# Kernel tuning notes

Hardware: AMD Instinct MI355X
Metric: run time of the kernel (lower is better)

Reference implementation:

```python
import jax, jax.numpy as jnp
import numpy as np

N_NODES = 50000
N_EDGES = 500000
H = 128          # h_dim
HEADS = 3
B = 512          # histories with non-zero length
L = 10           # seq_len (all histories full length)
N_RELS = 200
NEG_SLOPE = 0.2  # DGL GATConv default negative_slope


def setup_inputs() -> dict:
    key = jax.random.key(0)
    ks = jax.random.split(key, 18)
    p = lambda i, shape: jax.random.normal(ks[i], shape, jnp.float32) * 0.05
    return {
        "node_feat": jax.random.normal(ks[0], (N_NODES, H), jnp.float32),
        "W1": p(1, (H, HEADS * H)),
        "attn_l1": p(2, (HEADS, H)),
        "attn_r1": p(3, (HEADS, H)),
        "b1": p(4, (HEADS * H,)),
        "W2": p(5, (H, HEADS * H)),
        "attn_l2": p(6, (HEADS, H)),
        "attn_r2": p(7, (HEADS, H)),
        "b2": p(8, (HEADS * H,)),
        "ent_embeds": jax.random.normal(ks[9], (N_NODES, H), jnp.float32),
        "rel_embeds": jax.random.normal(ks[10], (N_RELS, H), jnp.float32),
        "global_emb_list": jax.random.normal(ks[11], (B * L, H), jnp.float32),
        "s_hist_t": jax.random.uniform(ks[12], (B, L), jnp.float32),
        "edge_src": jax.random.randint(ks[13], (N_EDGES,), 0, N_NODES),
        "edge_dst": jax.random.randint(ks[14], (N_EDGES,), 0, N_NODES),
        "node_ids_graph": jax.random.randint(ks[15], (B * L,), 0, N_NODES),
        "s_tem": jax.random.randint(ks[16], (B,), 0, N_NODES),
        "r_tem": jax.random.randint(ks[17], (B,), 0, N_RELS),
    }


def gat_conv(x, W, attn_l, attn_r, bias, src, dst):
    """DGL-style GATConv (allow_zero_in_degree=True, eval mode)."""
    n = x.shape[0]
    feat = (x @ W).reshape(n, HEADS, H)                    # [N, heads, H]
    el = jnp.einsum('nhd,hd->nh', feat, attn_l)            # [N, heads]
    er = jnp.einsum('nhd,hd->nh', feat, attn_r)
    e = jax.nn.leaky_relu(el[src] + er[dst], NEG_SLOPE)    # [E, heads]
    # edge softmax over incoming edges of each dst node
    emax = jax.ops.segment_max(e, dst, num_segments=n)
    ex = jnp.exp(e - emax[dst])
    denom = jax.ops.segment_sum(ex, dst, num_segments=n)
    alpha = ex / denom[dst]                                # [E, heads]
    msg = alpha[:, :, None] * feat[src]                    # [E, heads, H]
    rst = jax.ops.segment_sum(msg, dst, num_segments=n)    # [N, heads, H]
    return rst + bias.reshape(1, HEADS, H)


def reference(node_feat, W1, attn_l1, attn_r1, b1, W2, attn_l2, attn_r2, b2,
              ent_embeds, rel_embeds, global_emb_list, s_hist_t,
              edge_src, edge_dst, node_ids_graph, s_tem, r_tem):
    h = gat_conv(node_feat, W1, attn_l1, attn_r1, b1, edge_src, edge_dst).mean(axis=1)
    h = gat_conv(h, W2, attn_l2, attn_r2, b2, edge_src, edge_dst).mean(axis=1)
    embeds = h[node_ids_graph].reshape(B, L, H)            # gathered history node embeds
    ent = jnp.broadcast_to(ent_embeds[s_tem][:, None, :], (B, L, H))
    rel = jnp.broadcast_to(rel_embeds[r_tem][:, None, :], (B, L, H))
    glob = global_emb_list.reshape(B, L, H)
    seq = jnp.concatenate([embeds, ent, rel, glob], axis=-1)   # [B, L, 4H]
    seq_r = jnp.concatenate([embeds, ent, glob], axis=-1)      # [B, L, 3H]
    return seq, seq_r, s_hist_t
```

## Files before the change

### kernel.cpp

```cpp
#include <hip/hip_runtime.h>
#include <hip/hip_bf16.h>

#define N_NODES 50000
#define N_EDGES 500000
#define HDIM 128
#define HEADS 3
#define BB 512
#define LL 10
#define NEG_SLOPE 0.2f

typedef __hip_bfloat16 bf16;
typedef unsigned char fp8t;
typedef __bf16 v8bf __attribute__((ext_vector_type(8)));
typedef float f32x4 __attribute__((ext_vector_type(4)));


__global__ void k_zero2(int* a, int na, int* b, int nb){
  int i = blockIdx.x*256 + threadIdx.x;
  if(i < na) a[i] = 0;
  if(i < nb) b[i] = 0;
}

__global__ void k_hist(const int* __restrict__ dst, int* __restrict__ cnt, int E){
  int e = blockIdx.x*256 + threadIdx.x;
  if(e < E) atomicAdd(&cnt[dst[e]], 1);
}

__global__ void k_cvt(const float* __restrict__ in, bf16* __restrict__ o, int n){
  int i = (blockIdx.x*256 + threadIdx.x)*8;
  if(i < n){
    f32x4 lo = *reinterpret_cast<const f32x4*>(in + i);
    f32x4 hi = *reinterpret_cast<const f32x4*>(in + i + 4);
    v8bf v;
    #pragma unroll
    for(int j = 0; j < 4; ++j){ v[j] = (__bf16)lo[j]; v[4+j] = (__bf16)hi[j]; }
    *reinterpret_cast<v8bf*>(o + i) = v;
  }
}


#define SCAN_TILE 2048
#define SCAN_NB ((N_NODES + SCAN_TILE - 1)/SCAN_TILE)

__global__ __launch_bounds__(256) void k_scan_part(const int* __restrict__ cnt,
                                                   int* __restrict__ bsum){
  int b = blockIdx.x, tid = threadIdx.x;
  int i0 = b*SCAN_TILE + tid*8;
  int s = 0;
  #pragma unroll
  for(int j = 0; j < 8; ++j){ int i = i0 + j; s += (i < N_NODES) ? cnt[i] : 0; }
  for(int m = 32; m; m >>= 1) s += __shfl_xor(s, m);
  __shared__ int ws[4];
  if((tid & 63) == 0) ws[tid >> 6] = s;
  __syncthreads();
  if(tid == 0) bsum[b] = ws[0] + ws[1] + ws[2] + ws[3];
}

__global__ __launch_bounds__(64) void k_scan_top(int* __restrict__ bsum, int nb){
  int tid = threadIdx.x;
  int v = (tid < nb) ? bsum[tid] : 0;
  for(int s = 1; s < 64; s <<= 1){
    int t = __shfl_up(v, s);
    if(tid >= s) v += t;
  }
  if(tid < nb) bsum[tid] = v;
}

__global__ __launch_bounds__(256) void k_scan_write(int* __restrict__ cnt,
                                                    const int* __restrict__ bsum,
                                                    int* __restrict__ offs){
  int b = blockIdx.x, tid = threadIdx.x;
  int lane = tid & 63, wv = tid >> 6;
  int i0 = b*SCAN_TILE + tid*8;
  int v[8]; int s = 0;
  #pragma unroll
  for(int j = 0; j < 8; ++j){
    int i = i0 + j;
    v[j] = (i < N_NODES) ? cnt[i] : 0;
    s += v[j];
  }
  #pragma unroll
  for(int j = 0; j < 8; ++j){ int i = i0 + j; if(i < N_NODES) cnt[i] = 0; }
  int incl = s;
  for(int sh = 1; sh < 64; sh <<= 1){
    int t = __shfl_up(incl, sh);
    if(lane >= sh) incl += t;
  }
  __shared__ int wtot[4];
  if(lane == 63) wtot[wv] = incl;
  __syncthreads();
  int woff = 0;
  for(int w = 0; w < wv; ++w) woff += wtot[w];
  int excl = woff + incl - s;
  int run = ((b > 0) ? bsum[b-1] : 0) + excl;
  #pragma unroll
  for(int j = 0; j < 8; ++j){
    int i = i0 + j;
    run += v[j];
    if(i < N_NODES) offs[i+1] = run;
  }
  if(b == 0 && tid == 0) offs[0] = 0;
}

__global__ void k_scatter(const int* __restrict__ src, const int* __restrict__ dst,
                          const int* __restrict__ offs, int* __restrict__ cur,
                          int* __restrict__ csr, int E){
  int e = blockIdx.x*256 + threadIdx.x;
  if(e < E){
    int d = dst[e];
    int p = offs[d] + atomicAdd(&cur[d], 1);
    if(p >= 0 && p < E) csr[p] = src[e];
  }
}


__global__ __launch_bounds__(64) void k_mark(const int* __restrict__ nid,
                                             const int* __restrict__ offs,
                                             const int* __restrict__ csr,
                                             unsigned char* __restrict__ mark){
  unsigned n = (unsigned)nid[blockIdx.x];
  if(n >= N_NODES) return;
  if(threadIdx.x == 0) mark[n] = 1;
  int o0 = offs[n], o1 = offs[n+1];
  for(int j = o0 + (int)threadIdx.x; j < o1; j += 64){
    unsigned s = (unsigned)csr[j];
    if(s < N_NODES) mark[s] = 1;
  }
}


__global__ void k_wt(const float* __restrict__ W, bf16* __restrict__ Wt){
  int i = blockIdx.x*256 + threadIdx.x;
  if(i < HEADS*HDIM*HDIM){
    int n = i >> 7, k = i & 127;
    Wt[i] = __float2bfloat16(W[k*(HEADS*HDIM) + n]);
  }
}


__global__ __launch_bounds__(256) void k_gemm(const bf16* __restrict__ A,
                                              const bf16* __restrict__ Wt,
                                              const float* __restrict__ al,
                                              const float* __restrict__ ar,
                                              fp8t* __restrict__ feat8,
                                              float* __restrict__ el4,
                                              float* __restrict__ er4, int M){
  int tid  = threadIdx.x;
  int wave = tid >> 6, lane = tid & 63;
  int wr = wave >> 1, wc = wave & 1;
  int row0 = blockIdx.x*64 + wr*32;
  int col0 = blockIdx.y*128 + wc*64;
  int l15 = lane & 15, lhi = lane >> 4;

  v8bf a[4][2], b[4][4];
  #pragma unroll
  for(int kk = 0; kk < 4; ++kk){
    int kb = kk*32 + lhi*8;
    #pragma unroll
    for(int mi = 0; mi < 2; ++mi){
      int r = row0 + mi*16 + l15;
      if(r >= M) r = M - 1;
      a[kk][mi] = *reinterpret_cast<const v8bf*>(A + (size_t)r*HDIM + kb);
    }
    #pragma unroll
    for(int ni = 0; ni < 4; ++ni){
      int c = col0 + ni*16 + l15;
      b[kk][ni] = *reinterpret_cast<const v8bf*>(Wt + (size_t)c*HDIM + kb);
    }
  }

  f32x4 acc[2][4] = {};
  #pragma unroll
  for(int kk = 0; kk < 4; ++kk)
    #pragma unroll
    for(int mi = 0; mi < 2; ++mi)
      #pragma unroll
      for(int ni = 0; ni < 4; ++ni)
        acc[mi][ni] = __builtin_amdgcn_mfma_f32_16x16x32_bf16(a[kk][mi], b[kk][ni],
                                                              acc[mi][ni], 0, 0, 0);

  const float* alh = al + blockIdx.y*HDIM;
  const float* arh = ar + blockIdx.y*HDIM;
  float alv[4], arv[4];
  #pragma unroll
  for(int ni = 0; ni < 4; ++ni){
    int d = wc*64 + ni*16 + l15;
    alv[ni] = alh[d]; arv[ni] = arh[d];
  }
  __shared__ float red[2][64][2];
  __shared__ int4 tile4[512];
  fp8t* tile8 = (fp8t*)tile4;

  #pragma unroll
  for(int mi = 0; mi < 2; ++mi){
    #pragma unroll
    for(int j = 0; j < 4; ++j){
      float pe = 0.f, pr = 0.f;
      #pragma unroll
      for(int ni = 0; ni < 4; ++ni){
        pe += acc[mi][ni][j]*alv[ni];
        pr += acc[mi][ni][j]*arv[ni];
      }
      for(int k = 8; k; k >>= 1){ pe += __shfl_xor(pe, k); pr += __shfl_xor(pr, k); }
      int row_l = wr*32 + mi*16 + lhi*4 + j;
      if(l15 == 0){ red[wc][row_l][0] = pe; red[wc][row_l][1] = pr; }
    }
  }
  #pragma unroll
  for(int mi = 0; mi < 2; ++mi)
    #pragma unroll
    for(int j = 0; j < 4; ++j){
      int row_l = wr*32 + mi*16 + lhi*4 + j;
      #pragma unroll
      for(int ni = 0; ni < 4; ++ni){
        float x = acc[mi][ni][j];
        unsigned bb = (unsigned)__builtin_amdgcn_cvt_pk_fp8_f32(x, x, 0, false) & 0xFFu;
        tile8[row_l*128 + wc*64 + ni*16 + l15] = (fp8t)bb;
      }
    }
  __syncthreads();

  if(tid < 64){
    int r = blockIdx.x*64 + tid;
    if(r < M){
      el4[(size_t)r*4 + blockIdx.y] = red[0][tid][0] + red[1][tid][0];
      er4[(size_t)r*4 + blockIdx.y] = red[0][tid][1] + red[1][tid][1];
    }
  }
  #pragma unroll
  for(int pass = 0; pass < 2; ++pass){
    int off = pass*4096 + tid*16;
    int row_l = off >> 7, col = off & 127;
    int r = blockIdx.x*64 + row_l;
    if(r < M)
      *reinterpret_cast<int4*>(feat8 + (size_t)r*(HEADS*HDIM) + blockIdx.y*HDIM + col) =
          tile4[off >> 4];
  }
}


__device__ __forceinline__ float lrelu(float x){ return x > 0.f ? x : NEG_SLOPE*x; }

#define AGG_CHUNK 128
#define SEQ_SZ   (BB*LL*4*HDIM)
#define SEQR_OFF SEQ_SZ
#define SEQR_SZ  (BB*LL*3*HDIM)
#define SH_OFF   (SEQ_SZ + SEQR_SZ)

template<int USE_LIST, int FUSED, int USE_MARK>
__global__ __launch_bounds__(128) void k_agg(const fp8t* __restrict__ feat8,
                                             const float* __restrict__ el4,
                                             const float* __restrict__ er4,
                                             const float* __restrict__ bias,
                                             const int* __restrict__ offs,
                                             const int* __restrict__ csr,
                                             const int* __restrict__ list,
                                             const unsigned char* __restrict__ mark,
                                             bf16* __restrict__ h1,
                                             const float* __restrict__ ent_e,
                                             const float* __restrict__ rel_e,
                                             const float* __restrict__ glob,
                                             const float* __restrict__ sht,
                                             const int* __restrict__ s_tem,
                                             const int* __restrict__ r_tem,
                                             float* __restrict__ out){
  int bid = blockIdx.x;
  int n = USE_LIST ? list[bid] : bid;
  if(USE_MARK){ if(!mark[n]) return; }
  int tid = threadIdx.x;
  __shared__ float s_alpha[AGG_CHUNK][4];
  __shared__ int   s_src[AGG_CHUNK];
  __shared__ float s_facc[HEADS*HDIM];
  int o0 = offs[n];
  int deg = offs[n+1] - o0;
  if(deg < 0 || deg > N_EDGES) deg = 0;
  float4 erv = *reinterpret_cast<const float4*>(er4 + (size_t)n*4);

  float a0 = 0.f, a1 = 0.f, a2 = 0.f, a3 = 0.f, dh = 0.f;
  int head = tid >> 5;
  for(int base = 0; base < deg; base += AGG_CHUNK){
    int cn = min(AGG_CHUNK, deg - base);
    if(base) __syncthreads();
    if(tid < cn){
      unsigned su = (unsigned)csr[o0 + base + tid];
      if(su >= N_NODES) su = 0;
      float4 elv = *reinterpret_cast<const float4*>(el4 + (size_t)su*4);
      s_src[tid] = (int)su;
      s_alpha[tid][0] = __expf(lrelu(elv.x + erv.x));
      s_alpha[tid][1] = __expf(lrelu(elv.y + erv.y));
      s_alpha[tid][2] = __expf(lrelu(elv.z + erv.z));
    }
    __syncthreads();
    if(tid < 96){
      for(int i = 0; i < cn; ++i){
        unsigned u = *reinterpret_cast<const unsigned*>(
            feat8 + (size_t)s_src[i]*(HEADS*HDIM) + tid*4);
        float al = s_alpha[i][head];
        dh += al;
        a0 += al*__builtin_amdgcn_cvt_f32_fp8((int)u, 0);
        a1 += al*__builtin_amdgcn_cvt_f32_fp8((int)u, 1);
        a2 += al*__builtin_amdgcn_cvt_f32_fp8((int)u, 2);
        a3 += al*__builtin_amdgcn_cvt_f32_fp8((int)u, 3);
      }
    }
  }
  if(tid < 96){
    float inv = (dh > 0.f) ? 1.f/dh : 0.f;
    float4 w; w.x = a0*inv; w.y = a1*inv; w.z = a2*inv; w.w = a3*inv;
    *reinterpret_cast<float4*>(s_facc + tid*4) = w;
  }
  __syncthreads();
  float r = (s_facc[tid] + s_facc[HDIM + tid] + s_facc[2*HDIM + tid]
           + bias[tid] + bias[HDIM + tid] + bias[2*HDIM + tid])*(1.f/3.f);
  if(FUSED){
    int p = bid, b = p/LL, d = tid;
    float ent = ent_e[(size_t)s_tem[b]*HDIM + d];
    float rel = rel_e[(size_t)r_tem[b]*HDIM + d];
    float gl  = glob[(size_t)p*HDIM + d];
    size_t so = (size_t)p*(4*HDIM);
    out[so + d] = r; out[so + HDIM + d] = ent;
    out[so + 2*HDIM + d] = rel; out[so + 3*HDIM + d] = gl;
    size_t ro = SEQR_OFF + (size_t)p*(3*HDIM);
    out[ro + d] = r; out[ro + HDIM + d] = ent; out[ro + 2*HDIM + d] = gl;
    if(d == 0) out[SH_OFF + p] = sht[p];
  } else {
    h1[(size_t)n*HDIM + tid] = __float2bfloat16(r);
  }
}


extern "C" void kernel_launch(void* const* d_in, const int* in_sizes, int n_in,
                              void* d_out, int out_size, void* d_ws, size_t ws_size,
                              hipStream_t stream){
  const float* node_feat = (const float*)d_in[0];
  const float* W1        = (const float*)d_in[1];
  const float* attn_l1   = (const float*)d_in[2];
  const float* attn_r1   = (const float*)d_in[3];
  const float* b1        = (const float*)d_in[4];
  const float* W2        = (const float*)d_in[5];
  const float* attn_l2   = (const float*)d_in[6];
  const float* attn_r2   = (const float*)d_in[7];
  const float* b2        = (const float*)d_in[8];
  const float* ent_emb   = (const float*)d_in[9];
  const float* rel_emb   = (const float*)d_in[10];
  const float* glob      = (const float*)d_in[11];
  const float* sht       = (const float*)d_in[12];
  const int*  e_src      = (const int*)d_in[13];
  const int*  e_dst      = (const int*)d_in[14];
  const int*  nid        = (const int*)d_in[15];
  const int*  s_tem      = (const int*)d_in[16];
  const int*  r_tem      = (const int*)d_in[17];
  float* out = (float*)d_out;

  char* ws = (char*)d_ws;
  size_t cur_off = 0;
  auto alloc = [&](size_t bytes)->char*{
    char* r = ws + cur_off;
    cur_off += (bytes + 255) & ~(size_t)255;
    return r;
  };
  fp8t*  feat8 = (fp8t*) alloc((size_t)N_NODES*HEADS*HDIM);
  bf16*  nfb   = (bf16*) alloc((size_t)N_NODES*HDIM*2);
  bf16*  h1    = (bf16*) alloc((size_t)N_NODES*HDIM*2);
  float* el4   = (float*)alloc((size_t)N_NODES*4*4);
  float* er4   = (float*)alloc((size_t)N_NODES*4*4);
  bf16*  wt1   = (bf16*) alloc((size_t)HEADS*HDIM*HDIM*2);
  bf16*  wt2   = (bf16*) alloc((size_t)HEADS*HDIM*HDIM*2);
  int*   offs  = (int*)  alloc((size_t)(N_NODES+1)*4);
  int*   cnt   = (int*)  alloc((size_t)N_NODES*4);
  int*   bsum  = (int*)  alloc((size_t)SCAN_NB*4);
  unsigned char* mark = (unsigned char*)alloc((size_t)N_NODES);
  int*   csr   = (int*)  alloc((size_t)N_EDGES*4);

  k_zero2<<<(N_NODES+255)/256, 256, 0, stream>>>(cnt, N_NODES,
                                                 (int*)mark, (N_NODES+3)/4);
  k_hist<<<(N_EDGES+255)/256, 256, 0, stream>>>(e_dst, cnt, N_EDGES);
  k_scan_part<<<SCAN_NB, 256, 0, stream>>>(cnt, bsum);
  k_scan_top<<<1, 64, 0, stream>>>(bsum, SCAN_NB);
  k_scan_write<<<SCAN_NB, 256, 0, stream>>>(cnt, bsum, offs);
  k_scatter<<<(N_EDGES+255)/256, 256, 0, stream>>>(e_src, e_dst, offs, cnt, csr, N_EDGES);
  k_mark<<<BB*LL, 64, 0, stream>>>(nid, offs, csr, mark);

  k_wt<<<(HEADS*HDIM*HDIM+255)/256, 256, 0, stream>>>(W1, wt1);
  k_wt<<<(HEADS*HDIM*HDIM+255)/256, 256, 0, stream>>>(W2, wt2);
  k_cvt<<<(N_NODES*HDIM/8+255)/256, 256, 0, stream>>>(node_feat, nfb, N_NODES*HDIM);

  dim3 ggrid((N_NODES + 63)/64, HEADS);

  k_gemm<<<ggrid, 256, 0, stream>>>(nfb, wt1, attn_l1, attn_r1,
                                    feat8, el4, er4, N_NODES);
  k_agg<0,0,1><<<N_NODES, 128, 0, stream>>>(feat8, el4, er4, b1, offs, csr,
                                            nullptr, mark, h1,
                                            nullptr, nullptr, nullptr, nullptr,
                                            nullptr, nullptr, nullptr);

  k_gemm<<<ggrid, 256, 0, stream>>>(h1, wt2, attn_l2, attn_r2,
                                    feat8, el4, er4, N_NODES);
  k_agg<1,1,0><<<BB*LL, 128, 0, stream>>>(feat8, el4, er4, b2, offs, csr,
                                          nid, nullptr, nullptr,
                                          ent_emb, rel_emb, glob, sht,
                                          s_tem, r_tem, out);
}
```

Baseline: 197.4 us.

## Compact marked nodes for layer-2 GEMM and use wave-per-node aggregation

Builds a compacted list of the nodes needed by the final gather, from the existing mark array, using an atomic counter. The second-layer GEMM then computes projections only for those listed rows and exits early for blocks beyond the count. The aggregation kernel is also rewritten from one 128-thread block per node with shared-memory staging and barriers to one 64-lane wave per node, with four waves per block. Per-edge weights are broadcast through wave shuffles and the output uses vectorized stores. The compaction costs an extra kernel and an atomic, and list order is nondeterministic but only changes which row goes where.

```diff
diff --git a/kernel.cpp b/kernel.cpp
--- a/kernel.cpp
+++ b/kernel.cpp
@@ -15,10 +15,11 @@
 typedef float f32x4 __attribute__((ext_vector_type(4)));
 
 
-__global__ void k_zero2(int* a, int na, int* b, int nb){
+__global__ void k_zero2(int* a, int na, int* b, int nb, int* c){
   int i = blockIdx.x*256 + threadIdx.x;
   if(i < na) a[i] = 0;
   if(i < nb) b[i] = 0;
+  if(i == 0) c[0] = 0;
 }
 
 __global__ void k_hist(const int* __restrict__ dst, int* __restrict__ cnt, int E){
@@ -128,6 +129,15 @@
   }
 }
 
+__global__ void k_mklist(const unsigned char* __restrict__ mark,
+                         int* __restrict__ list, int* __restrict__ cnt){
+  int i = blockIdx.x*256 + threadIdx.x;
+  if(i < N_NODES && mark[i]){
+    int p = atomicAdd(cnt, 1);
+    list[p] = i;
+  }
+}
+
 
 __global__ void k_wt(const float* __restrict__ W, bf16* __restrict__ Wt){
   int i = blockIdx.x*256 + threadIdx.x;
@@ -138,13 +148,19 @@
 }
 
 
+template<int LIST>
 __global__ __launch_bounds__(256) void k_gemm(const bf16* __restrict__ A,
                                               const bf16* __restrict__ Wt,
                                               const float* __restrict__ al,
                                               const float* __restrict__ ar,
                                               fp8t* __restrict__ feat8,
                                               float* __restrict__ el4,
-                                              float* __restrict__ er4, int M){
+                                              float* __restrict__ er4,
+                                              const int* __restrict__ list,
+                                              const int* __restrict__ pcnt,
+                                              int M){
+  int Meff = LIST ? pcnt[0] : M;
+  if(blockIdx.x*64 >= Meff) return;
   int tid  = threadIdx.x;
   int wave = tid >> 6, lane = tid & 63;
   int wr = wave >> 1, wc = wave & 1;
@@ -153,15 +169,19 @@
   int l15 = lane & 15, lhi = lane >> 4;
 
   v8bf a[4][2], b[4][4];
+  int nodeA[2];
+  #pragma unroll
+  for(int mi = 0; mi < 2; ++mi){
+    int r = row0 + mi*16 + l15;
+    if(r >= Meff) r = Meff - 1;
+    nodeA[mi] = LIST ? list[r] : r;
+  }
   #pragma unroll
   for(int kk = 0; kk < 4; ++kk){
     int kb = kk*32 + lhi*8;
     #pragma unroll
-    for(int mi = 0; mi < 2; ++mi){
-      int r = row0 + mi*16 + l15;
-      if(r >= M) r = M - 1;
-      a[kk][mi] = *reinterpret_cast<const v8bf*>(A + (size_t)r*HDIM + kb);
-    }
+    for(int mi = 0; mi < 2; ++mi)
+      a[kk][mi] = *reinterpret_cast<const v8bf*>(A + (size_t)nodeA[mi]*HDIM + kb);
     #pragma unroll
     for(int ni = 0; ni < 4; ++ni){
       int c = col0 + ni*16 + l15;
@@ -222,9 +242,10 @@
 
   if(tid < 64){
     int r = blockIdx.x*64 + tid;
-    if(r < M){
-      el4[(size_t)r*4 + blockIdx.y] = red[0][tid][0] + red[1][tid][0];
-      er4[(size_t)r*4 + blockIdx.y] = red[0][tid][1] + red[1][tid][1];
+    if(r < Meff){
+      int node = LIST ? list[r] : r;
+      el4[(size_t)node*4 + blockIdx.y] = red[0][tid][0] + red[1][tid][0];
+      er4[(size_t)node*4 + blockIdx.y] = red[0][tid][1] + red[1][tid][1];
     }
   }
   #pragma unroll
@@ -232,23 +253,24 @@
     int off = pass*4096 + tid*16;
     int row_l = off >> 7, col = off & 127;
     int r = blockIdx.x*64 + row_l;
-    if(r < M)
-      *reinterpret_cast<int4*>(feat8 + (size_t)r*(HEADS*HDIM) + blockIdx.y*HDIM + col) =
+    if(r < Meff){
+      int node = LIST ? list[r] : r;
+      *reinterpret_cast<int4*>(feat8 + (size_t)node*(HEADS*HDIM) + blockIdx.y*HDIM + col) =
           tile4[off >> 4];
+    }
   }
 }
 
 
 __device__ __forceinline__ float lrelu(float x){ return x > 0.f ? x : NEG_SLOPE*x; }
 
-#define AGG_CHUNK 128
 #define SEQ_SZ   (BB*LL*4*HDIM)
 #define SEQR_OFF SEQ_SZ
 #define SEQR_SZ  (BB*LL*3*HDIM)
 #define SH_OFF   (SEQ_SZ + SEQR_SZ)
 
 template<int USE_LIST, int FUSED, int USE_MARK>
-__global__ __launch_bounds__(128) void k_agg(const fp8t* __restrict__ feat8,
+__global__ __launch_bounds__(256) void k_agg(const fp8t* __restrict__ feat8,
                                              const float* __restrict__ el4,
                                              const float* __restrict__ er4,
                                              const float* __restrict__ bias,
@@ -263,68 +285,100 @@
                                              const float* __restrict__ sht,
                                              const int* __restrict__ s_tem,
                                              const int* __restrict__ r_tem,
-                                             float* __restrict__ out){
-  int bid = blockIdx.x;
-  int n = USE_LIST ? list[bid] : bid;
+                                             float* __restrict__ out,
+                                             int total){
+  int widx = blockIdx.x*4 + (threadIdx.x >> 6);
+  int lane = threadIdx.x & 63;
+  if(widx >= total) return;
+  int n = USE_LIST ? list[widx] : widx;
   if(USE_MARK){ if(!mark[n]) return; }
-  int tid = threadIdx.x;
-  __shared__ float s_alpha[AGG_CHUNK][4];
-  __shared__ int   s_src[AGG_CHUNK];
-  __shared__ float s_facc[HEADS*HDIM];
   int o0 = offs[n];
   int deg = offs[n+1] - o0;
   if(deg < 0 || deg > N_EDGES) deg = 0;
   float4 erv = *reinterpret_cast<const float4*>(er4 + (size_t)n*4);
 
-  float a0 = 0.f, a1 = 0.f, a2 = 0.f, a3 = 0.f, dh = 0.f;
-  int head = tid >> 5;
-  for(int base = 0; base < deg; base += AGG_CHUNK){
-    int cn = min(AGG_CHUNK, deg - base);
-    if(base) __syncthreads();
-    if(tid < cn){
-      unsigned su = (unsigned)csr[o0 + base + tid];
+  float aA0=0.f,aA1=0.f,aA2=0.f,aA3=0.f, dhA=0.f;
+  float aB0=0.f,aB1=0.f,aB2=0.f,aB3=0.f, dhB=0.f;
+  int headA = lane >> 5;
+
+  for(int base = 0; base < deg; base += 64){
+    int cn = min(64, deg - base);
+    float e0 = 0.f, e1 = 0.f, e2 = 0.f; int s = 0;
+    if(lane < cn){
+      unsigned su = (unsigned)csr[o0 + base + lane];
       if(su >= N_NODES) su = 0;
+      s = (int)su;
       float4 elv = *reinterpret_cast<const float4*>(el4 + (size_t)su*4);
-      s_src[tid] = (int)su;
-      s_alpha[tid][0] = __expf(lrelu(elv.x + erv.x));
-      s_alpha[tid][1] = __expf(lrelu(elv.y + erv.y));
-      s_alpha[tid][2] = __expf(lrelu(elv.z + erv.z));
-    }
-    __syncthreads();
-    if(tid < 96){
-      for(int i = 0; i < cn; ++i){
-        unsigned u = *reinterpret_cast<const unsigned*>(
-            feat8 + (size_t)s_src[i]*(HEADS*HDIM) + tid*4);
-        float al = s_alpha[i][head];
-        dh += al;
-        a0 += al*__builtin_amdgcn_cvt_f32_fp8((int)u, 0);
-        a1 += al*__builtin_amdgcn_cvt_f32_fp8((int)u, 1);
-        a2 += al*__builtin_amdgcn_cvt_f32_fp8((int)u, 2);
-        a3 += al*__builtin_amdgcn_cvt_f32_fp8((int)u, 3);
+      e0 = __expf(lrelu(elv.x + erv.x));
+      e1 = __expf(lrelu(elv.y + erv.y));
+      e2 = __expf(lrelu(elv.z + erv.z));
+    }
+    for(int i = 0; i < cn; ++i){
+      int  si = __shfl(s,  i);
+      float b0 = __shfl(e0, i);
+      float b1 = __shfl(e1, i);
+      float b2 = __shfl(e2, i);
+      const fp8t* fr = feat8 + (size_t)si*(HEADS*HDIM);
+      unsigned uA = *reinterpret_cast<const unsigned*>(fr + lane*4);
+      float alA = headA ? b1 : b0;
+      dhA += alA;
+      aA0 += alA*__builtin_amdgcn_cvt_f32_fp8((int)uA, 0);
+      aA1 += alA*__builtin_amdgcn_cvt_f32_fp8((int)uA, 1);
+      aA2 += alA*__builtin_amdgcn_cvt_f32_fp8((int)uA, 2);
+      aA3 += alA*__builtin_amdgcn_cvt_f32_fp8((int)uA, 3);
+      if(lane < 32){
+        unsigned uB = *reinterpret_cast<const unsigned*>(fr + 256 + lane*4);
+        dhB += b2;
+        aB0 += b2*__builtin_amdgcn_cvt_f32_fp8((int)uB, 0);
+        aB1 += b2*__builtin_amdgcn_cvt_f32_fp8((int)uB, 1);
+        aB2 += b2*__builtin_amdgcn_cvt_f32_fp8((int)uB, 2);
+        aB3 += b2*__builtin_amdgcn_cvt_f32_fp8((int)uB, 3);
       }
     }
   }
-  if(tid < 96){
-    float inv = (dh > 0.f) ? 1.f/dh : 0.f;
-    float4 w; w.x = a0*inv; w.y = a1*inv; w.z = a2*inv; w.w = a3*inv;
-    *reinterpret_cast<float4*>(s_facc + tid*4) = w;
-  }
-  __syncthreads();
-  float r = (s_facc[tid] + s_facc[HDIM + tid] + s_facc[2*HDIM + tid]
-           + bias[tid] + bias[HDIM + tid] + bias[2*HDIM + tid])*(1.f/3.f);
-  if(FUSED){
-    int p = bid, b = p/LL, d = tid;
-    float ent = ent_e[(size_t)s_tem[b]*HDIM + d];
-    float rel = rel_e[(size_t)r_tem[b]*HDIM + d];
-    float gl  = glob[(size_t)p*HDIM + d];
-    size_t so = (size_t)p*(4*HDIM);
-    out[so + d] = r; out[so + HDIM + d] = ent;
-    out[so + 2*HDIM + d] = rel; out[so + 3*HDIM + d] = gl;
-    size_t ro = SEQR_OFF + (size_t)p*(3*HDIM);
-    out[ro + d] = r; out[ro + HDIM + d] = ent; out[ro + 2*HDIM + d] = gl;
-    if(d == 0) out[SH_OFF + p] = sht[p];
-  } else {
-    h1[(size_t)n*HDIM + tid] = __float2bfloat16(r);
+
+  float invA = (dhA > 0.f) ? 1.f/dhA : 0.f;
+  float invB = (dhB > 0.f) ? 1.f/dhB : 0.f;
+  float nA0 = aA0*invA, nA1 = aA1*invA, nA2 = aA2*invA, nA3 = aA3*invA;
+  float x0 = __shfl(nA0, lane + 32);
+  float x1 = __shfl(nA1, lane + 32);
+  float x2 = __shfl(nA2, lane + 32);
+  float x3 = __shfl(nA3, lane + 32);
+  if(lane < 32){
+    int m = lane;
+    float4 bs0 = *reinterpret_cast<const float4*>(bias + 4*m);
+    float4 bs1 = *reinterpret_cast<const float4*>(bias + HDIM + 4*m);
+    float4 bs2 = *reinterpret_cast<const float4*>(bias + 2*HDIM + 4*m);
+    float4 r;
+    r.x = (nA0 + x0 + aB0*invB + bs0.x + bs1.x + bs2.x)*(1.f/3.f);
+    r.y = (nA1 + x1 + aB1*invB + bs0.y + bs1.y + bs2.y)*(1.f/3.f);
+    r.z = (nA2 + x2 + aB2*invB + bs0.z + bs1.z + bs2.z)*(1.f/3.f);
+    r.w = (nA3 + x3 + aB3*invB + bs0.w + bs1.w + bs2.w)*(1.f/3.f);
+    if(FUSED){
+      int p = widx, bb = p/LL;
+      float4 ent = *reinterpret_cast<const float4*>(ent_e + (size_t)s_tem[bb]*HDIM + 4*m);
+      float4 rel = *reinterpret_cast<const float4*>(rel_e + (size_t)r_tem[bb]*HDIM + 4*m);
+      float4 gl  = *reinterpret_cast<const float4*>(glob + (size_t)p*HDIM + 4*m);
+      float* so = out + (size_t)p*(4*HDIM) + 4*m;
+      *reinterpret_cast<float4*>(so)            = r;
+      *reinterpret_cast<float4*>(so + HDIM)     = ent;
+      *reinterpret_cast<float4*>(so + 2*HDIM)   = rel;
+      *reinterpret_cast<float4*>(so + 3*HDIM)   = gl;
+      float* ro = out + SEQR_OFF + (size_t)p*(3*HDIM) + 4*m;
+      *reinterpret_cast<float4*>(ro)            = r;
+      *reinterpret_cast<float4*>(ro + HDIM)     = ent;
+      *reinterpret_cast<float4*>(ro + 2*HDIM)   = gl;
+      if(m == 0) out[SH_OFF + p] = sht[p];
+    } else {
+      bf16 t0 = __float2bfloat16(r.x), t1 = __float2bfloat16(r.y);
+      bf16 t2 = __float2bfloat16(r.z), t3 = __float2bfloat16(r.w);
+      ushort4 hv;
+      hv.x = *reinterpret_cast<unsigned short*>(&t0);
+      hv.y = *reinterpret_cast<unsigned short*>(&t1);
+      hv.z = *reinterpret_cast<unsigned short*>(&t2);
+      hv.w = *reinterpret_cast<unsigned short*>(&t3);
+      *reinterpret_cast<ushort4*>(h1 + (size_t)n*HDIM + 4*m) = hv;
+    }
   }
 }
 
@@ -370,16 +424,19 @@
   int*   cnt   = (int*)  alloc((size_t)N_NODES*4);
   int*   bsum  = (int*)  alloc((size_t)SCAN_NB*4);
   unsigned char* mark = (unsigned char*)alloc((size_t)N_NODES);
+  int*   mlist = (int*)  alloc((size_t)N_NODES*4);
+  int*   mcnt  = (int*)  alloc(256);
   int*   csr   = (int*)  alloc((size_t)N_EDGES*4);
 
   k_zero2<<<(N_NODES+255)/256, 256, 0, stream>>>(cnt, N_NODES,
-                                                 (int*)mark, (N_NODES+3)/4);
+                                                 (int*)mark, (N_NODES+3)/4, mcnt);
   k_hist<<<(N_EDGES+255)/256, 256, 0, stream>>>(e_dst, cnt, N_EDGES);
   k_scan_part<<<SCAN_NB, 256, 0, stream>>>(cnt, bsum);
   k_scan_top<<<1, 64, 0, stream>>>(bsum, SCAN_NB);
   k_scan_write<<<SCAN_NB, 256, 0, stream>>>(cnt, bsum, offs);
   k_scatter<<<(N_EDGES+255)/256, 256, 0, stream>>>(e_src, e_dst, offs, cnt, csr, N_EDGES);
   k_mark<<<BB*LL, 64, 0, stream>>>(nid, offs, csr, mark);
+  k_mklist<<<(N_NODES+255)/256, 256, 0, stream>>>(mark, mlist, mcnt);
 
   k_wt<<<(HEADS*HDIM*HDIM+255)/256, 256, 0, stream>>>(W1, wt1);
   k_wt<<<(HEADS*HDIM*HDIM+255)/256, 256, 0, stream>>>(W2, wt2);
@@ -387,17 +444,17 @@
 
   dim3 ggrid((N_NODES + 63)/64, HEADS);
 
-  k_gemm<<<ggrid, 256, 0, stream>>>(nfb, wt1, attn_l1, attn_r1,
-                                    feat8, el4, er4, N_NODES);
-  k_agg<0,0,1><<<N_NODES, 128, 0, stream>>>(feat8, el4, er4, b1, offs, csr,
-                                            nullptr, mark, h1,
-                                            nullptr, nullptr, nullptr, nullptr,
-                                            nullptr, nullptr, nullptr);
-
-  k_gemm<<<ggrid, 256, 0, stream>>>(h1, wt2, attn_l2, attn_r2,
-                                    feat8, el4, er4, N_NODES);
-  k_agg<1,1,0><<<BB*LL, 128, 0, stream>>>(feat8, el4, er4, b2, offs, csr,
-                                          nid, nullptr, nullptr,
-                                          ent_emb, rel_emb, glob, sht,
-                                          s_tem, r_tem, out);
-}
+  k_gemm<0><<<ggrid, 256, 0, stream>>>(nfb, wt1, attn_l1, attn_r1,
+                                       feat8, el4, er4, nullptr, nullptr, N_NODES);
+  k_agg<0,0,1><<<(N_NODES+3)/4, 256, 0, stream>>>(feat8, el4, er4, b1, offs, csr,
+                                                  nullptr, mark, h1,
+                                                  nullptr, nullptr, nullptr, nullptr,
+                                                  nullptr, nullptr, nullptr, N_NODES);
+
+  k_gemm<1><<<ggrid, 256, 0, stream>>>(h1, wt2, attn_l2, attn_r2,
+                                       feat8, el4, er4, mlist, mcnt, N_NODES);
+  k_agg<1,1,0><<<(BB*LL+3)/4, 256, 0, stream>>>(feat8, el4, er4, b2, offs, csr,
+                                                nid, nullptr, nullptr,
+                                                ent_emb, rel_emb, glob, sht,
+                                                s_tem, r_tem, out, BB*LL);
+}
```

After: 210.0 us. 1.06x slower.

## Restrict second-layer GEMM to marked nodes via compacted list; unroll aggregation

Applied to the files above, without the earlier changes.

Builds a compacted list of marked nodes (history nodes and their in-neighbours) with an atomic counter. The second GEMM is then computed only for those rows, with early exit for tiles beyond the count. The GEMM grid is also remapped so consecutive blocks share a row group across heads, and the aggregation inner loop is unrolled by four so more gathers are in flight. This removes unneeded layer-2 GEMM work, at the cost of an extra kernel, atomic-ordered (non-deterministic) list order, and indirect row loads.

```diff
diff --git a/kernel.cpp b/kernel.cpp
--- a/kernel.cpp
+++ b/kernel.cpp
@@ -15,10 +15,11 @@
 typedef float f32x4 __attribute__((ext_vector_type(4)));
 
 
-__global__ void k_zero2(int* a, int na, int* b, int nb){
+__global__ void k_zero2(int* a, int na, int* b, int nb, int* c){
   int i = blockIdx.x*256 + threadIdx.x;
   if(i < na) a[i] = 0;
   if(i < nb) b[i] = 0;
+  if(i == 0) c[0] = 0;
 }
 
 __global__ void k_hist(const int* __restrict__ dst, int* __restrict__ cnt, int E){
@@ -128,6 +129,15 @@
   }
 }
 
+__global__ void k_mklist(const unsigned char* __restrict__ mark,
+                         int* __restrict__ list, int* __restrict__ cnt){
+  int i = blockIdx.x*256 + threadIdx.x;
+  if(i < N_NODES && mark[i]){
+    int p = atomicAdd(cnt, 1);
+    list[p] = i;
+  }
+}
+
 
 __global__ void k_wt(const float* __restrict__ W, bf16* __restrict__ Wt){
   int i = blockIdx.x*256 + threadIdx.x;
@@ -138,30 +148,46 @@
 }
 
 
+#define GEMM_NBR 784
+#define GEMM_GRID (GEMM_NBR/8*24)
+
+template<int LIST>
 __global__ __launch_bounds__(256) void k_gemm(const bf16* __restrict__ A,
                                               const bf16* __restrict__ Wt,
                                               const float* __restrict__ al,
                                               const float* __restrict__ ar,
                                               fp8t* __restrict__ feat8,
                                               float* __restrict__ el4,
-                                              float* __restrict__ er4, int M){
+                                              float* __restrict__ er4,
+                                              const int* __restrict__ list,
+                                              const int* __restrict__ pcnt,
+                                              int M){
+  int g = blockIdx.x/24, o = blockIdx.x - g*24;
+  int rt = g*8 + (o & 7);
+  int head = o >> 3;
+  int Meff = LIST ? pcnt[0] : M;
+  if(rt*64 >= Meff) return;
   int tid  = threadIdx.x;
   int wave = tid >> 6, lane = tid & 63;
   int wr = wave >> 1, wc = wave & 1;
-  int row0 = blockIdx.x*64 + wr*32;
-  int col0 = blockIdx.y*128 + wc*64;
+  int row0 = rt*64 + wr*32;
+  int col0 = head*128 + wc*64;
   int l15 = lane & 15, lhi = lane >> 4;
 
   v8bf a[4][2], b[4][4];
+  int nodeA[2];
+  #pragma unroll
+  for(int mi = 0; mi < 2; ++mi){
+    int r = row0 + mi*16 + l15;
+    if(r >= Meff) r = Meff - 1;
+    nodeA[mi] = LIST ? list[r] : r;
+  }
   #pragma unroll
   for(int kk = 0; kk < 4; ++kk){
     int kb = kk*32 + lhi*8;
     #pragma unroll
-    for(int mi = 0; mi < 2; ++mi){
-      int r = row0 + mi*16 + l15;
-      if(r >= M) r = M - 1;
-      a[kk][mi] = *reinterpret_cast<const v8bf*>(A + (size_t)r*HDIM + kb);
-    }
+    for(int mi = 0; mi < 2; ++mi)
+      a[kk][mi] = *reinterpret_cast<const v8bf*>(A + (size_t)nodeA[mi]*HDIM + kb);
     #pragma unroll
     for(int ni = 0; ni < 4; ++ni){
       int c = col0 + ni*16 + l15;
@@ -179,8 +205,8 @@
         acc[mi][ni] = __builtin_amdgcn_mfma_f32_16x16x32_bf16(a[kk][mi], b[kk][ni],
                                                               acc[mi][ni], 0, 0, 0);
 
-  const float* alh = al + blockIdx.y*HDIM;
-  const float* arh = ar + blockIdx.y*HDIM;
+  const float* alh = al + head*HDIM;
+  const float* arh = ar + head*HDIM;
   float alv[4], arv[4];
   #pragma unroll
   for(int ni = 0; ni < 4; ++ni){
@@ -221,20 +247,23 @@
   __syncthreads();
 
   if(tid < 64){
-    int r = blockIdx.x*64 + tid;
-    if(r < M){
-      el4[(size_t)r*4 + blockIdx.y] = red[0][tid][0] + red[1][tid][0];
-      er4[(size_t)r*4 + blockIdx.y] = red[0][tid][1] + red[1][tid][1];
+    int r = rt*64 + tid;
+    if(r < Meff){
+      int node = LIST ? list[r] : r;
+      el4[(size_t)node*4 + head] = red[0][tid][0] + red[1][tid][0];
+      er4[(size_t)node*4 + head] = red[0][tid][1] + red[1][tid][1];
     }
   }
   #pragma unroll
   for(int pass = 0; pass < 2; ++pass){
     int off = pass*4096 + tid*16;
     int row_l = off >> 7, col = off & 127;
-    int r = blockIdx.x*64 + row_l;
-    if(r < M)
-      *reinterpret_cast<int4*>(feat8 + (size_t)r*(HEADS*HDIM) + blockIdx.y*HDIM + col) =
+    int r = rt*64 + row_l;
+    if(r < Meff){
+      int node = LIST ? list[r] : r;
+      *reinterpret_cast<int4*>(feat8 + (size_t)node*(HEADS*HDIM) + head*HDIM + col) =
           tile4[off >> 4];
+    }
   }
 }
 
@@ -292,7 +321,39 @@
     }
     __syncthreads();
     if(tid < 96){
-      for(int i = 0; i < cn; ++i){
+      int i = 0;
+      for(; i + 4 <= cn; i += 4){
+        unsigned u0 = *reinterpret_cast<const unsigned*>(
+            feat8 + (size_t)s_src[i+0]*(HEADS*HDIM) + tid*4);
+        unsigned u1 = *reinterpret_cast<const unsigned*>(
+            feat8 + (size_t)s_src[i+1]*(HEADS*HDIM) + tid*4);
+        unsigned u2 = *reinterpret_cast<const unsigned*>(
+            feat8 + (size_t)s_src[i+2]*(HEADS*HDIM) + tid*4);
+        unsigned u3 = *reinterpret_cast<const unsigned*>(
+            feat8 + (size_t)s_src[i+3]*(HEADS*HDIM) + tid*4);
+        float al0 = s_alpha[i+0][head];
+        float al1 = s_alpha[i+1][head];
+        float al2 = s_alpha[i+2][head];
+        float al3 = s_alpha[i+3][head];
+        dh += al0 + al1 + al2 + al3;
+        a0 += al0*__builtin_amdgcn_cvt_f32_fp8((int)u0, 0)
+            + al1*__builtin_amdgcn_cvt_f32_fp8((int)u1, 0)
+            + al2*__builtin_amdgcn_cvt_f32_fp8((int)u2, 0)
+            + al3*__builtin_amdgcn_cvt_f32_fp8((int)u3, 0);
+        a1 += al0*__builtin_amdgcn_cvt_f32_fp8((int)u0, 1)
+            + al1*__builtin_amdgcn_cvt_f32_fp8((int)u1, 1)
+            + al2*__builtin_amdgcn_cvt_f32_fp8((int)u2, 1)
+            + al3*__builtin_amdgcn_cvt_f32_fp8((int)u3, 1);
+        a2 += al0*__builtin_amdgcn_cvt_f32_fp8((int)u0, 2)
+            + al1*__builtin_amdgcn_cvt_f32_fp8((int)u1, 2)
+            + al2*__builtin_amdgcn_cvt_f32_fp8((int)u2, 2)
+            + al3*__builtin_amdgcn_cvt_f32_fp8((int)u3, 2);
+        a3 += al0*__builtin_amdgcn_cvt_f32_fp8((int)u0, 3)
+            + al1*__builtin_amdgcn_cvt_f32_fp8((int)u1, 3)
+            + al2*__builtin_amdgcn_cvt_f32_fp8((int)u2, 3)
+            + al3*__builtin_amdgcn_cvt_f32_fp8((int)u3, 3);
+      }
+      for(; i < cn; ++i){
         unsigned u = *reinterpret_cast<const unsigned*>(
             feat8 + (size_t)s_src[i]*(HEADS*HDIM) + tid*4);
         float al = s_alpha[i][head];
@@ -370,32 +431,33 @@
   int*   cnt   = (int*)  alloc((size_t)N_NODES*4);
   int*   bsum  = (int*)  alloc((size_t)SCAN_NB*4);
   unsigned char* mark = (unsigned char*)alloc((size_t)N_NODES);
+  int*   mlist = (int*)  alloc((size_t)N_NODES*4);
+  int*   mcnt  = (int*)  alloc(256);
   int*   csr   = (int*)  alloc((size_t)N_EDGES*4);
 
   k_zero2<<<(N_NODES+255)/256, 256, 0, stream>>>(cnt, N_NODES,
-                                                 (int*)mark, (N_NODES+3)/4);
+                                                 (int*)mark, (N_NODES+3)/4, mcnt);
   k_hist<<<(N_EDGES+255)/256, 256, 0, stream>>>(e_dst, cnt, N_EDGES);
   k_scan_part<<<SCAN_NB, 256, 0, stream>>>(cnt, bsum);
   k_scan_top<<<1, 64, 0, stream>>>(bsum, SCAN_NB);
   k_scan_write<<<SCAN_NB, 256, 0, stream>>>(cnt, bsum, offs);
   k_scatter<<<(N_EDGES+255)/256, 256, 0, stream>>>(e_src, e_dst, offs, cnt, csr, N_EDGES);
   k_mark<<<BB*LL, 64, 0, stream>>>(nid, offs, csr, mark);
+  k_mklist<<<(N_NODES+255)/256, 256, 0, stream>>>(mark, mlist, mcnt);
 
   k_wt<<<(HEADS*HDIM*HDIM+255)/256, 256, 0, stream>>>(W1, wt1);
   k_wt<<<(HEADS*HDIM*HDIM+255)/256, 256, 0, stream>>>(W2, wt2);
   k_cvt<<<(N_NODES*HDIM/8+255)/256, 256, 0, stream>>>(node_feat, nfb, N_NODES*HDIM);
 
-  dim3 ggrid((N_NODES + 63)/64, HEADS);
-
-  k_gemm<<<ggrid, 256, 0, stream>>>(nfb, wt1, attn_l1, attn_r1,
-                                    feat8, el4, er4, N_NODES);
+  k_gemm<0><<<GEMM_GRID, 256, 0, stream>>>(nfb, wt1, attn_l1, attn_r1,
+                                           feat8, el4, er4, nullptr, nullptr, N_NODES);
   k_agg<0,0,1><<<N_NODES, 128, 0, stream>>>(feat8, el4, er4, b1, offs, csr,
                                             nullptr, mark, h1,
                                             nullptr, nullptr, nullptr, nullptr,
                                             nullptr, nullptr, nullptr);
 
-  k_gemm<<<ggrid, 256, 0, stream>>>(h1, wt2, attn_l2, attn_r2,
-                                    feat8, el4, er4, N_NODES);
+  k_gemm<1><<<GEMM_GRID, 256, 0, stream>>>(h1, wt2, attn_l2, attn_r2,
+                                           feat8, el4, er4, mlist, mcnt, N_NODES);
   k_agg<1,1,0><<<BB*LL, 128, 0, stream>>>(feat8, el4, er4, b2, offs, csr,
                                           nid, nullptr, nullptr,
                                           ent_emb, rel_emb, glob, sht,
```

Result: slower. 201.7 us (+2.2%).
